# Optimization experiments

Hardware: AMD Instinct MI355X
Metric: run time of the kernel (lower is better)

## Reference

```python
import jax, jax.numpy as jnp
import numpy as np
import math

B, QL, KL, H, QD, KD, VD = 4, 1024, 1024, 16, 1024, 1024, 1024
QH = QD // H  # 64
KH = KD // H  # 64


def setup_inputs() -> dict:
    rng = jax.random.key(0)
    ks = jax.random.split(rng, 8)
    return {
        "query": jax.random.normal(ks[0], (B, QL, QD), jnp.float32),
        "key": jax.random.normal(ks[1], (B, KL, KD), jnp.float32),
        "value": jax.random.normal(ks[2], (B, KL, VD), jnp.float32),
        "pad_mask": jax.random.randint(ks[3], (B, QL), 0, 2),
        "q_w": jax.random.uniform(ks[4], (H, QL, QH), jnp.float32),
        "k_w": jax.random.uniform(ks[5], (H, KL, KH), jnp.float32),
        "v_w": jax.random.uniform(ks[6], (H, KL, KH), jnp.float32),
        "o_w": jax.random.uniform(ks[7], (H * KH, QD), jnp.float32),
    }


def reference(query, key, value, pad_mask, q_w, k_w, v_w, o_w):
    b = query.shape[0]
    h, ql, qh = q_w.shape
    kl, kh = k_w.shape[1], k_w.shape[2]

    # mask construction: causal (triu, offset 1) OR pad mask tiled as in torch repeat+view
    causal = jnp.triu(jnp.ones((ql, kl), jnp.float32), 1) == 1            # [i, j]
    pad = jnp.tile(pad_mask, (1, kl)).reshape(b, ql, kl) == 1             # [b, i, j]
    mask = causal[None, :, :] | pad                                      # [b, i, j]

    # positional per-head projections: free index of input feature dim is summed out
    wq = jnp.einsum('biq,his->bhis', query, q_w)                          # [b, h, i, s]
    wk = jnp.einsum('bjk,hjt->bhjt', key, k_w)                            # [b, h, j, t]
    wv = jnp.einsum('bjv,hjt->bhjt', value, v_w)                          # [b, h, j, t]

    scale = math.sqrt(h)  # torch uses query.size()[1] == head_num after projection
    scores = jnp.einsum('bhis,bhjs->bhij', wq, wk) / scale                # [b, h, i, j]
    scores = jnp.where(mask[:, None, :, :], -jnp.inf, scores)
    scores = jnp.nan_to_num(scores)  # -inf -> finfo.min, matching torch.nan_to_num

    weight = jax.nn.softmax(scores, axis=0)  # unusual: softmax over the batch axis
    heads = jnp.einsum('bhij,bhjt->bhit', weight, wv)                     # [b, h, i, t]
    heads = heads.reshape(b, -1, h * kh)  # torch .view: reinterprets [h,i,t] as [i, h*t]
    return jnp.einsum('bit,to->bio', heads, o_w)                          # [b, i, q_dim]
```

## Files before the change

kernel.cpp:

```cpp
#include <hip/hip_runtime.h>
#include <hip/hip_bf16.h>

#define NB 4
#define NL 1024
#define NH 16
#define ND 1024
#define HD 64
#define FMIN_F32 (-3.4028234663852886e38f)
#define LOG2E 1.4426950408889634f

typedef __bf16 bf16x8 __attribute__((ext_vector_type(8)));
typedef float f32x4 __attribute__((ext_vector_type(4)));
typedef unsigned int u32;

static __device__ inline unsigned short f2bf(float f) {
    __hip_bfloat16 h = __float2bfloat16(f);
    return __builtin_bit_cast(unsigned short, h);
}

static __device__ inline void bfsplit(float x, unsigned short& hi, unsigned short& lo) {
    unsigned u = __builtin_bit_cast(unsigned, x);
    unsigned r = (u + 0x7FFFu + ((u >> 16) & 1u)) >> 16;
    hi = (unsigned short)r;
    float hf = __builtin_bit_cast(float, r << 16);
    lo = f2bf(x - hf);
}

static __device__ __forceinline__ void gload16(void* lds, const void* g) {
    __builtin_amdgcn_global_load_lds(
        (const __attribute__((address_space(1))) u32*)g,
        (__attribute__((address_space(3))) u32*)lds, 16, 0, 0);
}

__global__ __launch_bounds__(256)
void rowsum_kernel(const float* __restrict__ q, const float* __restrict__ k,
                   const float* __restrict__ v, float* __restrict__ out) {
    int gw   = blockIdx.x * 4 + (threadIdx.x >> 6);
    int lane = threadIdx.x & 63;
    int tensor = gw >> 12;
    int row    = gw & 4095;
    const float* src = tensor == 0 ? q : (tensor == 1 ? k : v);
    const float* p = src + (size_t)row * ND;
    float s = 0.f;
#pragma unroll
    for (int t = 0; t < 4; ++t) {
        float4 x = *reinterpret_cast<const float4*>(p + t * 256 + lane * 4);
        s += (x.x + x.y) + (x.z + x.w);
    }
#pragma unroll
    for (int off = 32; off; off >>= 1) s += __shfl_xor(s, off);
    if (lane == 0) out[tensor * (NB * NL) + row] = s;
}

__global__ __launch_bounds__(256)
void prep_kernel(const float* __restrict__ k_w, const float* __restrict__ v_w,
                 const float* __restrict__ o_w, const float* __restrict__ sums,
                 unsigned short* __restrict__ kPhi, unsigned short* __restrict__ kPlo,
                 unsigned short* __restrict__ vP, unsigned short* __restrict__ BP,
                 float* __restrict__ S) {
    __shared__ float tile[64][132];
    __shared__ float vsL[256];
    const int tid = threadIdx.x;
    const int bx  = blockIdx.x;
    if (bx < 256) {
        const int h = bx >> 4, jt = bx & 15;
        char* hiT = (char*)kPhi + (size_t)(h * 16 + jt) * 8192;
        char* loT = (char*)kPlo + (size_t)(h * 16 + jt) * 8192;
        const int row = tid >> 2;
        const int s0  = (tid & 3) * 16;
        const float* src = k_w + ((size_t)(h * NL + jt * 64 + row)) * HD + s0;
#pragma unroll
        for (int t = 0; t < 4; ++t) {
            float4 x = reinterpret_cast<const float4*>(src)[t];
            unsigned short h0, h1, h2, h3, l0, l1, l2, l3;
            bfsplit(x.x, h0, l0); bfsplit(x.y, h1, l1);
            bfsplit(x.z, h2, l2); bfsplit(x.w, h3, l3);
            int off = (row * 128 + (s0 + 4 * t) * 2) ^ ((row & 7) << 4);
            *(uint2*)(hiT + off) = make_uint2((u32)h0 | ((u32)h1 << 16),
                                              (u32)h2 | ((u32)h3 << 16));
            *(uint2*)(loT + off) = make_uint2((u32)l0 | ((u32)l1 << 16),
                                              (u32)l2 | ((u32)l3 << 16));
        }
    } else if (bx < 512) {
        const int h = (bx - 256) >> 4, jt = (bx - 256) & 15;
#pragma unroll
        for (int t = 0; t < 4; ++t) {
            int id = tid + 256 * t;
            int j = id >> 4, t4 = (id & 15) * 4;
            *(float4*)&tile[j][t4] =
                *(const float4*)(v_w + ((size_t)(h * NL + jt * 64 + j)) * HD + t4);
        }
        vsL[tid] = sums[2 * NB * NL + (tid >> 6) * NL + jt * 64 + (tid & 63)];
        __syncthreads();
        char* vT_ = (char*)vP + (size_t)(h * 16 + jt) * 8192;
        const int trow = tid >> 2;
        const int jq   = (tid & 3) * 16;
#pragma unroll
        for (int q = 0; q < 4; ++q) {
            int j4 = jq + 4 * q;
            uint2 u;
            u.x = (u32)f2bf(tile[j4 + 0][trow]) | ((u32)f2bf(tile[j4 + 1][trow]) << 16);
            u.y = (u32)f2bf(tile[j4 + 2][trow]) | ((u32)f2bf(tile[j4 + 3][trow]) << 16);
            int off = (trow * 128 + j4 * 2) ^ ((trow & 7) << 4);
            *(uint2*)(vT_ + off) = u;
        }
        if (jt >= 1) {
            const int b = tid >> 6, t = tid & 63;
            float a = 0.f;
#pragma unroll 16
            for (int j = 0; j < 64; ++j)
                a = fmaf(vsL[b * 64 + j], tile[j][t], a);
            S[(((size_t)h * 16 + jt) * 4 + b) * 64 + t] = a;
        }
    } else {
        const int bxo = bx - 512;
        const int ot = bxo >> 4, kt = bxo & 15;
#pragma unroll
        for (int t = 0; t < 8; ++t) {
            int id = tid + 256 * t;
            int c = id >> 5, o4 = (id & 31) * 4;
            *(float4*)&tile[c][o4] =
                *(const float4*)(o_w + ((size_t)(kt * 64 + c)) * ND + ot * 128 + o4);
        }
        __syncthreads();
        char* bT = (char*)BP + (size_t)(ot * 16 + kt) * 16384;
#pragma unroll
        for (int t = 0; t < 8; ++t) {
            int id = tid + 256 * t;
            int ol = id >> 4, c4 = (id & 15) * 4;
            uint2 u;
            u.x = (u32)f2bf(tile[c4 + 0][ol]) | ((u32)f2bf(tile[c4 + 1][ol]) << 16);
            u.y = (u32)f2bf(tile[c4 + 2][ol]) | ((u32)f2bf(tile[c4 + 3][ol]) << 16);
            int off = (ol * 128 + c4 * 2) ^ ((ol & 7) << 4);
            *(uint2*)(bT + off) = u;
        }
    }
}

__global__ __launch_bounds__(512, 4)
void attn_kernel(const float* __restrict__ q_w, const int* __restrict__ pad,
                 const float* __restrict__ sums,
                 const unsigned short* __restrict__ kPhi,
                 const unsigned short* __restrict__ kPlo,
                 const unsigned short* __restrict__ vP,
                 const float* __restrict__ S,
                 unsigned short* __restrict__ AP) {
    __shared__ __align__(16) unsigned short kHi[2][4096], kLo[2][4096], vTl[2][4096];
    __shared__ __align__(16) unsigned short qHi[2048], qLo[2048];
    __shared__ __align__(16) unsigned short wlds[8192];
    __shared__ __align__(16) float qs4[128];
    __shared__ __align__(16) float ks4[2][256];
    __shared__ __align__(16) float vs4[2][256];
    __shared__ __align__(16) int   pm4[2][256];

    const float* qsum = sums;
    const float* ksum = sums + NB * NL;
    const float* vsum = sums + 2 * NB * NL;

    const int wid = blockIdx.x;
    const int gq  = wid >> 4;
    const int h   = wid & 15;
    const int itp = (gq < 16) ? (2 * gq) : (63 - 2 * gq);
    const int it0 = itp * 32;
    const int cut = (it0 >> 6) + 1;

    const int tid  = threadIdx.x;
    const int lane = tid & 63;
    const int w    = tid >> 6;
    const int l15  = lane & 15;
    const int kb   = (lane >> 4) * 16;

    {
        int row = tid >> 4;
        int s4  = (tid & 15) * 4;
        float4 x = *(const float4*)(q_w + ((size_t)(h * NL + it0 + row)) * HD + s4);
        unsigned short h0, h1, h2, h3, l0, l1, l2, l3;
        bfsplit(x.x, h0, l0); bfsplit(x.y, h1, l1);
        bfsplit(x.z, h2, l2); bfsplit(x.w, h3, l3);
        int off = (row * 128 + s4 * 2) ^ ((row & 7) << 4);
        *(uint2*)((char*)qHi + off) = make_uint2((u32)h0 | ((u32)h1 << 16),
                                                 (u32)h2 | ((u32)h3 << 16));
        *(uint2*)((char*)qLo + off) = make_uint2((u32)l0 | ((u32)l1 << 16),
                                                 (u32)l2 | ((u32)l3 << 16));
    }
    if (tid < 128) {
        int b = tid >> 5, i = tid & 31;
        qs4[i * 4 + b] = qsum[b * NL + it0 + i];
    }

    auto stage = [&](int buf, int jt) {
        const size_t tb = (size_t)(h * 16 + jt) * 8192 + tid * 16;
        gload16((char*)kHi[buf] + tid * 16, (const char*)kPhi + tb);
        gload16((char*)kLo[buf] + tid * 16, (const char*)kPlo + tb);
        gload16((char*)vTl[buf] + tid * 16, (const char*)vP + tb);
        if (tid < 256) {
            int b = tid >> 6, jj = tid & 63;
            ks4[buf][jj * 4 + b] = ksum[b * NL + jt * 64 + jj] * (LOG2E * 0.25f);
            vs4[buf][jj * 4 + b] = vsum[b * NL + jt * 64 + jj];
            pm4[buf][jj * 4 + b] = pad[b * NL + jt * 64 + jj];
        }
    };

    const int gmi = (w & 1) * 16;
    const int gnj = (w >> 1) * 16;
    const int pb  = w >> 1;
    const int pmh = (w & 1) * 16;

    f32x4 accP[4];
#pragma unroll
    for (int n = 0; n < 4; ++n) accP[n] = (f32x4){0.f, 0.f, 0.f, 0.f};

    stage(0, 0);
    __syncthreads();
    int cur = 0;

    const int i_sm  = gmi + l15;
    const int ig    = it0 + i_sm;
    const int jb_sm = gnj + (lane >> 4) * 4;
    const float4 qsv = *(const float4*)&qs4[i_sm * 4];
    const int woff = (i_sm * 128 + jb_sm * 2) ^ ((i_sm & 7) << 4);

    for (int jt = 0; jt < cut; ++jt) {
        const int j0 = jt * 64;
        if (jt + 1 < cut) stage(cur ^ 1, jt + 1);

        f32x4 g = (f32x4){0.f, 0.f, 0.f, 0.f};
#pragma unroll
        for (int ks = 0; ks < 2; ++ks) {
            const int arow = gnj + l15;
            const int brow = gmi + l15;
            const int aoff = (arow * 128 + ks * 64 + kb) ^ ((arow & 7) << 4);
            const int boff = (brow * 128 + ks * 64 + kb) ^ ((brow & 7) << 4);
            bf16x8 kHiF = __builtin_bit_cast(bf16x8, *(const uint4*)((const char*)kHi[cur] + aoff));
            bf16x8 kLoF = __builtin_bit_cast(bf16x8, *(const uint4*)((const char*)kLo[cur] + aoff));
            bf16x8 qHiF = __builtin_bit_cast(bf16x8, *(const uint4*)((const char*)qHi + boff));
            bf16x8 qLoF = __builtin_bit_cast(bf16x8, *(const uint4*)((const char*)qLo + boff));
            g = __builtin_amdgcn_mfma_f32_16x16x32_bf16(kHiF, qHiF, g, 0, 0, 0);
            g = __builtin_amdgcn_mfma_f32_16x16x32_bf16(kLoF, qHiF, g, 0, 0, 0);
            g = __builtin_amdgcn_mfma_f32_16x16x32_bf16(kHiF, qLoF, g, 0, 0, 0);
        }

        {
            float wv[4][4];
#pragma unroll
            for (int r = 0; r < 4; ++r) {
                const int j  = jb_sm + r;
                const int jg = j0 + j;
                const float4 ksv = *(const float4*)&ks4[cur][j * 4];
                const float4 vsv = *(const float4*)&vs4[cur][j * 4];
                const int4   pmv = *(const int4*)&pm4[cur][j * 4];
                const float gr = g[r];
                const bool causal = jg > ig;
                const float sb0 = (causal || pmv.x) ? FMIN_F32 : qsv.x * ksv.x * gr;
                const float sb1 = (causal || pmv.y) ? FMIN_F32 : qsv.y * ksv.y * gr;
                const float sb2 = (causal || pmv.z) ? FMIN_F32 : qsv.z * ksv.z * gr;
                const float sb3 = (causal || pmv.w) ? FMIN_F32 : qsv.w * ksv.w * gr;
                const float mx = fmaxf(fmaxf(sb0, sb1), fmaxf(sb2, sb3));
                const float e0 = __builtin_amdgcn_exp2f(sb0 - mx);
                const float e1 = __builtin_amdgcn_exp2f(sb1 - mx);
                const float e2 = __builtin_amdgcn_exp2f(sb2 - mx);
                const float e3 = __builtin_amdgcn_exp2f(sb3 - mx);
                const float inv = __builtin_amdgcn_rcpf((e0 + e1) + (e2 + e3));
                wv[r][0] = e0 * inv * vsv.x;
                wv[r][1] = e1 * inv * vsv.y;
                wv[r][2] = e2 * inv * vsv.z;
                wv[r][3] = e3 * inv * vsv.w;
            }
#pragma unroll
            for (int b = 0; b < 4; ++b) {
                uint2 p;
                p.x = (u32)f2bf(wv[0][b]) | ((u32)f2bf(wv[1][b]) << 16);
                p.y = (u32)f2bf(wv[2][b]) | ((u32)f2bf(wv[3][b]) << 16);
                *(uint2*)((char*)wlds + b * 4096 + woff) = p;
            }
        }
        asm volatile("s_waitcnt lgkmcnt(0)" ::: "memory");
        __builtin_amdgcn_s_barrier();
        __builtin_amdgcn_sched_barrier(0);

#pragma unroll
        for (int ks = 0; ks < 2; ++ks) {
            const int arow = pmh + l15;
            const int aoff = pb * 4096 + ((arow * 128 + ks * 64 + kb) ^ ((arow & 7) << 4));
            bf16x8 aF = __builtin_bit_cast(bf16x8, *(const uint4*)((const char*)wlds + aoff));
#pragma unroll
            for (int n = 0; n < 4; ++n) {
                const int vrow = n * 16 + l15;
                const int voff = (vrow * 128 + ks * 64 + kb) ^ ((vrow & 7) << 4);
                bf16x8 bF = __builtin_bit_cast(bf16x8, *(const uint4*)((const char*)vTl[cur] + voff));
                accP[n] = __builtin_amdgcn_mfma_f32_16x16x32_bf16(aF, bF, accP[n], 0, 0, 0);
            }
        }
        __syncthreads();
        cur ^= 1;
    }

    if (cut < 16) {
        float sv[4] = {0.f, 0.f, 0.f, 0.f};
        for (int jt = cut; jt < 16; ++jt) {
            const float* sp = S + (((size_t)h * 16 + jt) * 4 + pb) * 64;
#pragma unroll
            for (int n = 0; n < 4; ++n) sv[n] += sp[n * 16 + l15];
        }
#pragma unroll
        for (int n = 0; n < 4; ++n) {
            const float s4v = 0.25f * sv[n];
#pragma unroll
            for (int r = 0; r < 4; ++r) accP[n][r] += s4v;
        }
    }

    {
        const int ib = (it0 + pmh) >> 4;
        char* tbase = (char*)AP + (size_t)((pb * 16 + h) * 16) * 8192;
#pragma unroll
        for (int n = 0; n < 4; ++n)
#pragma unroll
            for (int r = 0; r < 4; ++r) {
                int kt = (lane >> 4) * 4 + r;
                int tt = n * 16 + l15;
                int off = (ib * 128 + tt * 2) ^ ((ib & 7) << 4);
                *(unsigned short*)(tbase + (size_t)kt * 8192 + off) = f2bf(accP[n][r]);
            }
    }
}

__global__ __launch_bounds__(256, 2)
void outgemm_kernel(const unsigned short* __restrict__ AP,
                    const unsigned short* __restrict__ BP,
                    float* __restrict__ out) {
    __shared__ __align__(16) unsigned short aL[3][4096];
    __shared__ __align__(16) unsigned short bL[3][8192];
    const int ox = blockIdx.x;
    const int my = blockIdx.y;
    const int tid  = threadIdx.x;
    const int lane = tid & 63;
    const int w    = tid >> 6;
    const int wr = (w & 1) * 32;
    const int wc = (w >> 1) * 64;
    const int l15  = lane & 15;
    const int kseg = (lane >> 4) * 16;

    f32x4 acc[2][4];
#pragma unroll
    for (int m = 0; m < 2; ++m)
#pragma unroll
        for (int n = 0; n < 4; ++n) acc[m][n] = (f32x4){0.f, 0.f, 0.f, 0.f};

    auto stage = [&](int buf, int kt) {
        const char* at = (const char*)AP + (size_t)(my * 16 + kt) * 8192;
        const char* bt = (const char*)BP + (size_t)(ox * 16 + kt) * 16384;
        gload16((char*)aL[buf] + tid * 16, at + tid * 16);
        gload16((char*)aL[buf] + 4096 + tid * 16, at + 4096 + tid * 16);
#pragma unroll
        for (int r = 0; r < 4; ++r)
            gload16((char*)bL[buf] + r * 4096 + tid * 16, bt + r * 4096 + tid * 16);
    };

    auto compute = [&](int cb) {
#pragma unroll
        for (int ks = 0; ks < 2; ++ks) {
            bf16x8 aF[2], bF[4];
#pragma unroll
            for (int m = 0; m < 2; ++m) {
                int row = wr + m * 16 + l15;
                int off = (row * 128 + ks * 64 + kseg) ^ ((row & 7) << 4);
                aF[m] = __builtin_bit_cast(bf16x8, *(const uint4*)((const char*)aL[cb] + off));
            }
#pragma unroll
            for (int n = 0; n < 4; ++n) {
                int row = wc + n * 16 + l15;
                int off = (row * 128 + ks * 64 + kseg) ^ ((row & 7) << 4);
                bF[n] = __builtin_bit_cast(bf16x8, *(const uint4*)((const char*)bL[cb] + off));
            }
#pragma unroll
            for (int m = 0; m < 2; ++m)
#pragma unroll
                for (int n = 0; n < 4; ++n)
                    acc[m][n] = __builtin_amdgcn_mfma_f32_16x16x32_bf16(
                        aF[m], bF[n], acc[m][n], 0, 0, 0);
        }
    };

    stage(0, 0);
    stage(1, 1);
    for (int kt = 0; kt < 15; ++kt) {
        asm volatile("s_waitcnt vmcnt(6)" ::: "memory");
        __builtin_amdgcn_s_barrier();
        __builtin_amdgcn_sched_barrier(0);
        if (kt + 2 < 16) stage((kt + 2) % 3, kt + 2);
        compute(kt % 3);
    }
    asm volatile("s_waitcnt vmcnt(0)" ::: "memory");
    __builtin_amdgcn_s_barrier();
    __builtin_amdgcn_sched_barrier(0);
    compute(15 % 3);

#pragma unroll
    for (int m = 0; m < 2; ++m)
#pragma unroll
        for (int n = 0; n < 4; ++n)
#pragma unroll
            for (int r = 0; r < 4; ++r) {
                int row = my * 64 + wr + m * 16 + (lane >> 4) * 4 + r;
                int col = ox * 128 + wc + n * 16 + l15;
                out[(size_t)row * ND + col] = acc[m][n][r];
            }
}

extern "C" void kernel_launch(void* const* d_in, const int* in_sizes, int n_in,
                              void* d_out, int out_size, void* d_ws, size_t ws_size,
                              hipStream_t stream) {
    const float* query = (const float*)d_in[0];
    const float* key   = (const float*)d_in[1];
    const float* value = (const float*)d_in[2];
    const int*   pad   = (const int*)d_in[3];
    const float* q_w   = (const float*)d_in[4];
    const float* k_w   = (const float*)d_in[5];
    const float* v_w   = (const float*)d_in[6];
    const float* o_w   = (const float*)d_in[7];
    float* out = (float*)d_out;

    char* W = (char*)d_ws;
    float*          sums = (float*)W;
    unsigned short* kPhi = (unsigned short*)(W + 49152);
    unsigned short* kPlo = (unsigned short*)(W + 2146304);
    unsigned short* vP   = (unsigned short*)(W + 4243456);
    unsigned short* BP   = (unsigned short*)(W + 6340608);
    unsigned short* AP   = (unsigned short*)(W + 8437760);

    float* S = out;

    rowsum_kernel<<<3 * (NB * NL) / 4, 256, 0, stream>>>(query, key, value, sums);

    prep_kernel<<<640, 256, 0, stream>>>(k_w, v_w, o_w, sums, kPhi, kPlo, vP, BP, S);

    attn_kernel<<<512, 512, 0, stream>>>(q_w, pad, sums, kPhi, kPlo, vP, S, AP);

    dim3 gg(8, 64);
    outgemm_kernel<<<gg, 256, 0, stream>>>(AP, BP, out);
}
```

Measured before the change: 69.19 us.

## Precompute per-key softmax factors and pad bitmask in prep; keep Q fragments in registers

```diff
diff --git a/kernel.cpp b/kernel.cpp
--- a/kernel.cpp
+++ b/kernel.cpp
@@ -24,6 +24,10 @@
     hi = (unsigned short)r;
     float hf = __builtin_bit_cast(float, r << 16);
     lo = f2bf(x - hf);
+}
+
+static __device__ inline u32 pk2(unsigned short a, unsigned short b) {
+    return (u32)a | ((u32)b << 16);
 }
 
 static __device__ __forceinline__ void gload16(void* lds, const void* g) {
@@ -55,13 +59,17 @@
 __global__ __launch_bounds__(256)
 void prep_kernel(const float* __restrict__ k_w, const float* __restrict__ v_w,
                  const float* __restrict__ o_w, const float* __restrict__ sums,
+                 const int* __restrict__ pad,
                  unsigned short* __restrict__ kPhi, unsigned short* __restrict__ kPlo,
                  unsigned short* __restrict__ vP, unsigned short* __restrict__ BP,
-                 float* __restrict__ S) {
+                 float* __restrict__ S, float* __restrict__ ksg,
+                 float* __restrict__ vsg, int* __restrict__ pmi) {
     __shared__ float tile[64][132];
     __shared__ float vsL[256];
     const int tid = threadIdx.x;
     const int bx  = blockIdx.x;
+    const float* ksum = sums + NB * NL;
+    const float* vsum = sums + 2 * NB * NL;
     if (bx < 256) {
         const int h = bx >> 4, jt = bx & 15;
         char* hiT = (char*)kPhi + (size_t)(h * 16 + jt) * 8192;
@@ -76,10 +84,8 @@
             bfsplit(x.x, h0, l0); bfsplit(x.y, h1, l1);
             bfsplit(x.z, h2, l2); bfsplit(x.w, h3, l3);
             int off = (row * 128 + (s0 + 4 * t) * 2) ^ ((row & 7) << 4);
-            *(uint2*)(hiT + off) = make_uint2((u32)h0 | ((u32)h1 << 16),
-                                              (u32)h2 | ((u32)h3 << 16));
-            *(uint2*)(loT + off) = make_uint2((u32)l0 | ((u32)l1 << 16),
-                                              (u32)l2 | ((u32)l3 << 16));
+            *(uint2*)(hiT + off) = make_uint2(pk2(h0, h1), pk2(h2, h3));
+            *(uint2*)(loT + off) = make_uint2(pk2(l0, l1), pk2(l2, l3));
         }
     } else if (bx < 512) {
         const int h = (bx - 256) >> 4, jt = (bx - 256) & 15;
@@ -90,7 +96,7 @@
             *(float4*)&tile[j][t4] =
                 *(const float4*)(v_w + ((size_t)(h * NL + jt * 64 + j)) * HD + t4);
         }
-        vsL[tid] = sums[2 * NB * NL + (tid >> 6) * NL + jt * 64 + (tid & 63)];
+        vsL[tid] = vsum[(tid >> 6) * NL + jt * 64 + (tid & 63)];
         __syncthreads();
         char* vT_ = (char*)vP + (size_t)(h * 16 + jt) * 8192;
         const int trow = tid >> 2;
@@ -99,8 +105,8 @@
         for (int q = 0; q < 4; ++q) {
             int j4 = jq + 4 * q;
             uint2 u;
-            u.x = (u32)f2bf(tile[j4 + 0][trow]) | ((u32)f2bf(tile[j4 + 1][trow]) << 16);
-            u.y = (u32)f2bf(tile[j4 + 2][trow]) | ((u32)f2bf(tile[j4 + 3][trow]) << 16);
+            u.x = pk2(f2bf(tile[j4 + 0][trow]), f2bf(tile[j4 + 1][trow]));
+            u.y = pk2(f2bf(tile[j4 + 2][trow]), f2bf(tile[j4 + 3][trow]));
             int off = (trow * 128 + j4 * 2) ^ ((trow & 7) << 4);
             *(uint2*)(vT_ + off) = u;
         }
@@ -112,7 +118,7 @@
                 a = fmaf(vsL[b * 64 + j], tile[j][t], a);
             S[(((size_t)h * 16 + jt) * 4 + b) * 64 + t] = a;
         }
-    } else {
+    } else if (bx < 640) {
         const int bxo = bx - 512;
         const int ot = bxo >> 4, kt = bxo & 15;
 #pragma unroll
@@ -129,33 +135,34 @@
             int id = tid + 256 * t;
             int ol = id >> 4, c4 = (id & 15) * 4;
             uint2 u;
-            u.x = (u32)f2bf(tile[c4 + 0][ol]) | ((u32)f2bf(tile[c4 + 1][ol]) << 16);
-            u.y = (u32)f2bf(tile[c4 + 2][ol]) | ((u32)f2bf(tile[c4 + 3][ol]) << 16);
+            u.x = pk2(f2bf(tile[c4 + 0][ol]), f2bf(tile[c4 + 1][ol]));
+            u.y = pk2(f2bf(tile[c4 + 2][ol]), f2bf(tile[c4 + 3][ol]));
             int off = (ol * 128 + c4 * 2) ^ ((ol & 7) << 4);
             *(uint2*)(bT + off) = u;
         }
+    } else {
+        const int e = (bx - 640) * 256 + tid;
+        const int j = e >> 2, b = e & 3;
+        ksg[e] = ksum[b * NL + j] * (LOG2E * 0.25f);
+        vsg[e] = vsum[b * NL + j];
+        if (b == 0)
+            pmi[j] = pad[j] | (pad[NL + j] << 1) | (pad[2 * NL + j] << 2) |
+                     (pad[3 * NL + j] << 3);
     }
 }
 
 __global__ __launch_bounds__(512, 4)
-void attn_kernel(const float* __restrict__ q_w, const int* __restrict__ pad,
-                 const float* __restrict__ sums,
+void attn_kernel(const float* __restrict__ q_w, const float* __restrict__ sums,
                  const unsigned short* __restrict__ kPhi,
                  const unsigned short* __restrict__ kPlo,
                  const unsigned short* __restrict__ vP,
-                 const float* __restrict__ S,
+                 const float* __restrict__ ksg, const float* __restrict__ vsg,
+                 const int* __restrict__ pmi, const float* __restrict__ S,
                  unsigned short* __restrict__ AP) {
     __shared__ __align__(16) unsigned short kHi[2][4096], kLo[2][4096], vTl[2][4096];
-    __shared__ __align__(16) unsigned short qHi[2048], qLo[2048];
     __shared__ __align__(16) unsigned short wlds[8192];
-    __shared__ __align__(16) float qs4[128];
-    __shared__ __align__(16) float ks4[2][256];
-    __shared__ __align__(16) float vs4[2][256];
-    __shared__ __align__(16) int   pm4[2][256];
 
     const float* qsum = sums;
-    const float* ksum = sums + NB * NL;
-    const float* vsum = sums + 2 * NB * NL;
 
     const int wid = blockIdx.x;
     const int gq  = wid >> 4;
@@ -170,41 +177,42 @@
     const int l15  = lane & 15;
     const int kb   = (lane >> 4) * 16;
 
+    const int gmi = (w & 1) * 16;
+    const int gnj = (w >> 1) * 16;
+    const int pb  = w >> 1;
+    const int pmh = (w & 1) * 16;
+
+    const int i_sm = gmi + l15;
+    const int ig   = it0 + i_sm;
+    bf16x8 qHiF[2], qLoF[2];
     {
-        int row = tid >> 4;
-        int s4  = (tid & 15) * 4;
-        float4 x = *(const float4*)(q_w + ((size_t)(h * NL + it0 + row)) * HD + s4);
-        unsigned short h0, h1, h2, h3, l0, l1, l2, l3;
-        bfsplit(x.x, h0, l0); bfsplit(x.y, h1, l1);
-        bfsplit(x.z, h2, l2); bfsplit(x.w, h3, l3);
-        int off = (row * 128 + s4 * 2) ^ ((row & 7) << 4);
-        *(uint2*)((char*)qHi + off) = make_uint2((u32)h0 | ((u32)h1 << 16),
-                                                 (u32)h2 | ((u32)h3 << 16));
-        *(uint2*)((char*)qLo + off) = make_uint2((u32)l0 | ((u32)l1 << 16),
-                                                 (u32)l2 | ((u32)l3 << 16));
-    }
-    if (tid < 128) {
-        int b = tid >> 5, i = tid & 31;
-        qs4[i * 4 + b] = qsum[b * NL + it0 + i];
-    }
+        const float* qp = q_w + ((size_t)(h * NL + ig)) * HD + (lane >> 4) * 8;
+#pragma unroll
+        for (int ks = 0; ks < 2; ++ks) {
+            float f[8];
+            *(float4*)&f[0] = *(const float4*)(qp + ks * 32);
+            *(float4*)&f[4] = *(const float4*)(qp + ks * 32 + 4);
+            unsigned short hh[8], ll[8];
+#pragma unroll
+            for (int e = 0; e < 8; ++e) bfsplit(f[e], hh[e], ll[e]);
+            uint4 H = make_uint4(pk2(hh[0], hh[1]), pk2(hh[2], hh[3]),
+                                 pk2(hh[4], hh[5]), pk2(hh[6], hh[7]));
+            uint4 L = make_uint4(pk2(ll[0], ll[1]), pk2(ll[2], ll[3]),
+                                 pk2(ll[4], ll[5]), pk2(ll[6], ll[7]));
+            qHiF[ks] = __builtin_bit_cast(bf16x8, H);
+            qLoF[ks] = __builtin_bit_cast(bf16x8, L);
+        }
+    }
+    float4 qsv;
+    qsv.x = qsum[0 * NL + ig]; qsv.y = qsum[1 * NL + ig];
+    qsv.z = qsum[2 * NL + ig]; qsv.w = qsum[3 * NL + ig];
 
     auto stage = [&](int buf, int jt) {
         const size_t tb = (size_t)(h * 16 + jt) * 8192 + tid * 16;
         gload16((char*)kHi[buf] + tid * 16, (const char*)kPhi + tb);
         gload16((char*)kLo[buf] + tid * 16, (const char*)kPlo + tb);
         gload16((char*)vTl[buf] + tid * 16, (const char*)vP + tb);
-        if (tid < 256) {
-            int b = tid >> 6, jj = tid & 63;
-            ks4[buf][jj * 4 + b] = ksum[b * NL + jt * 64 + jj] * (LOG2E * 0.25f);
-            vs4[buf][jj * 4 + b] = vsum[b * NL + jt * 64 + jj];
-            pm4[buf][jj * 4 + b] = pad[b * NL + jt * 64 + jj];
-        }
     };
-
-    const int gmi = (w & 1) * 16;
-    const int gnj = (w >> 1) * 16;
-    const int pb  = w >> 1;
-    const int pmh = (w & 1) * 16;
 
     f32x4 accP[4];
 #pragma unroll
@@ -214,47 +222,40 @@
     __syncthreads();
     int cur = 0;
 
-    const int i_sm  = gmi + l15;
-    const int ig    = it0 + i_sm;
     const int jb_sm = gnj + (lane >> 4) * 4;
-    const float4 qsv = *(const float4*)&qs4[i_sm * 4];
-    const int woff = (i_sm * 128 + jb_sm * 2) ^ ((i_sm & 7) << 4);
+    const int woff  = (i_sm * 128 + jb_sm * 2) ^ ((i_sm & 7) << 4);
 
     for (int jt = 0; jt < cut; ++jt) {
         const int j0 = jt * 64;
         if (jt + 1 < cut) stage(cur ^ 1, jt + 1);
 
-        f32x4 g = (f32x4){0.f, 0.f, 0.f, 0.f};
+        f32x4 gA = (f32x4){0.f, 0.f, 0.f, 0.f};
+        f32x4 gB = (f32x4){0.f, 0.f, 0.f, 0.f};
 #pragma unroll
         for (int ks = 0; ks < 2; ++ks) {
             const int arow = gnj + l15;
-            const int brow = gmi + l15;
             const int aoff = (arow * 128 + ks * 64 + kb) ^ ((arow & 7) << 4);
-            const int boff = (brow * 128 + ks * 64 + kb) ^ ((brow & 7) << 4);
             bf16x8 kHiF = __builtin_bit_cast(bf16x8, *(const uint4*)((const char*)kHi[cur] + aoff));
             bf16x8 kLoF = __builtin_bit_cast(bf16x8, *(const uint4*)((const char*)kLo[cur] + aoff));
-            bf16x8 qHiF = __builtin_bit_cast(bf16x8, *(const uint4*)((const char*)qHi + boff));
-            bf16x8 qLoF = __builtin_bit_cast(bf16x8, *(const uint4*)((const char*)qLo + boff));
-            g = __builtin_amdgcn_mfma_f32_16x16x32_bf16(kHiF, qHiF, g, 0, 0, 0);
-            g = __builtin_amdgcn_mfma_f32_16x16x32_bf16(kLoF, qHiF, g, 0, 0, 0);
-            g = __builtin_amdgcn_mfma_f32_16x16x32_bf16(kHiF, qLoF, g, 0, 0, 0);
-        }
+            gA = __builtin_amdgcn_mfma_f32_16x16x32_bf16(kHiF, qHiF[ks], gA, 0, 0, 0);
+            gA = __builtin_amdgcn_mfma_f32_16x16x32_bf16(kLoF, qHiF[ks], gA, 0, 0, 0);
+            gB = __builtin_amdgcn_mfma_f32_16x16x32_bf16(kHiF, qLoF[ks], gB, 0, 0, 0);
+        }
+        const f32x4 g = gA + gB;
 
         {
             float wv[4][4];
 #pragma unroll
             for (int r = 0; r < 4; ++r) {
-                const int j  = jb_sm + r;
-                const int jg = j0 + j;
-                const float4 ksv = *(const float4*)&ks4[cur][j * 4];
-                const float4 vsv = *(const float4*)&vs4[cur][j * 4];
-                const int4   pmv = *(const int4*)&pm4[cur][j * 4];
+                const int jg = j0 + jb_sm + r;
+                const float4 ksv = *(const float4*)(ksg + 4 * jg);
+                const float4 vsv = *(const float4*)(vsg + 4 * jg);
+                const int pm = pmi[jg] | ((jg > ig) ? 15 : 0);
                 const float gr = g[r];
-                const bool causal = jg > ig;
-                const float sb0 = (causal || pmv.x) ? FMIN_F32 : qsv.x * ksv.x * gr;
-                const float sb1 = (causal || pmv.y) ? FMIN_F32 : qsv.y * ksv.y * gr;
-                const float sb2 = (causal || pmv.z) ? FMIN_F32 : qsv.z * ksv.z * gr;
-                const float sb3 = (causal || pmv.w) ? FMIN_F32 : qsv.w * ksv.w * gr;
+                const float sb0 = (pm & 1) ? FMIN_F32 : qsv.x * ksv.x * gr;
+                const float sb1 = (pm & 2) ? FMIN_F32 : qsv.y * ksv.y * gr;
+                const float sb2 = (pm & 4) ? FMIN_F32 : qsv.z * ksv.z * gr;
+                const float sb3 = (pm & 8) ? FMIN_F32 : qsv.w * ksv.w * gr;
                 const float mx = fmaxf(fmaxf(sb0, sb1), fmaxf(sb2, sb3));
                 const float e0 = __builtin_amdgcn_exp2f(sb0 - mx);
                 const float e1 = __builtin_amdgcn_exp2f(sb1 - mx);
@@ -269,8 +270,8 @@
 #pragma unroll
             for (int b = 0; b < 4; ++b) {
                 uint2 p;
-                p.x = (u32)f2bf(wv[0][b]) | ((u32)f2bf(wv[1][b]) << 16);
-                p.y = (u32)f2bf(wv[2][b]) | ((u32)f2bf(wv[3][b]) << 16);
+                p.x = pk2(f2bf(wv[0][b]), f2bf(wv[1][b]));
+                p.y = pk2(f2bf(wv[2][b]), f2bf(wv[3][b]));
                 *(uint2*)((char*)wlds + b * 4096 + woff) = p;
             }
         }
@@ -278,6 +279,7 @@
         __builtin_amdgcn_s_barrier();
         __builtin_amdgcn_sched_barrier(0);
 
+        __builtin_amdgcn_s_setprio(1);
 #pragma unroll
         for (int ks = 0; ks < 2; ++ks) {
             const int arow = pmh + l15;
@@ -291,6 +293,7 @@
                 accP[n] = __builtin_amdgcn_mfma_f32_16x16x32_bf16(aF, bF, accP[n], 0, 0, 0);
             }
         }
+        __builtin_amdgcn_s_setprio(0);
         __syncthreads();
         cur ^= 1;
     }
@@ -358,6 +361,7 @@
     };
 
     auto compute = [&](int cb) {
+        __builtin_amdgcn_s_setprio(1);
 #pragma unroll
         for (int ks = 0; ks < 2; ++ks) {
             bf16x8 aF[2], bF[4];
@@ -380,6 +384,7 @@
                     acc[m][n] = __builtin_amdgcn_mfma_f32_16x16x32_bf16(
                         aF[m], bF[n], acc[m][n], 0, 0, 0);
         }
+        __builtin_amdgcn_s_setprio(0);
     };
 
     stage(0, 0);
@@ -428,14 +433,19 @@
     unsigned short* vP   = (unsigned short*)(W + 4243456);
     unsigned short* BP   = (unsigned short*)(W + 6340608);
     unsigned short* AP   = (unsigned short*)(W + 8437760);
+    float*          ksg  = (float*)(W + 16826368);
+    float*          vsg  = (float*)(W + 16842752);
+    int*            pmi  = (int*)(W + 16859136);
 
     float* S = out;
 
     rowsum_kernel<<<3 * (NB * NL) / 4, 256, 0, stream>>>(query, key, value, sums);
 
-    prep_kernel<<<640, 256, 0, stream>>>(k_w, v_w, o_w, sums, kPhi, kPlo, vP, BP, S);
-
-    attn_kernel<<<512, 512, 0, stream>>>(q_w, pad, sums, kPhi, kPlo, vP, S, AP);
+    prep_kernel<<<656, 256, 0, stream>>>(k_w, v_w, o_w, sums, pad,
+                                         kPhi, kPlo, vP, BP, S, ksg, vsg, pmi);
+
+    attn_kernel<<<512, 512, 0, stream>>>(q_w, sums, kPhi, kPlo, vP,
+                                         ksg, vsg, pmi, S, AP);
 
     dim3 gg(8, 64);
     outgemm_kernel<<<gg, 256, 0, stream>>>(AP, BP, out);
```

Result: slower. 75.67 us (+9.4%).
